# Kernel tuning notes

Hardware: AMD Instinct MI355X
Metric: run time of the kernel (lower is better)

Reference implementation:

```python
import jax, jax.numpy as jnp
import numpy as np

BLOCK = 32            # MX block size (base-class default)
FMT_MAX = 1.984375    # MXINT8 element max = 127/64 (concrete _quantize_elements choice)
QSTEP = 64.0          # quantization grid step 2^-6
BUDGET = 8.0          # cfg.msd_cycle_budget
THRESH = 0.0          # cfg.msd_budget_dynamic_threshold
ALPHA = 1.0           # cfg.msd_budget_dynamic_scale (mode='linear')
NEG = -60.0           # log2 sentinel for zero/negative values


def _safe_log2(x):
    return jnp.where(x > 0, jnp.log2(jnp.maximum(x, 1e-45)), NEG)


def _quantize_blocks(t):
    """Per-block shared fp32 scale + MXINT8-style element quantization.
    t: (rows, feat) with feat % BLOCK == 0 -> q (rows, nb, bs), scales (rows, nb)."""
    rows = t.shape[0]
    blocks = t.reshape(rows, -1, BLOCK)
    max_abs = jnp.max(jnp.abs(blocks), axis=-1)
    scales = jnp.maximum(max_abs / FMT_MAX, 1e-30)
    q = jnp.round(blocks / scales[..., None] * QSTEP) / QSTEP
    return q, scales


def _msd_truncate(value, num_digits):
    """Truncate each element to its num_digits most-significant NAF (BSD) digits."""
    abs_v = jnp.abs(value)
    sign = jnp.sign(value)
    mask = (num_digits > 0) & (abs_v > 0)
    msb_pos = jnp.floor(jnp.log2(jnp.maximum(abs_v, 1e-45)))
    scale_up = jnp.exp2(23.0 - msb_pos)              # place MSB at bit 23
    x_scaled = jnp.round(abs_v * scale_up).astype(jnp.int32)
    x_h = x_scaled >> 1
    s = x_scaled + x_h
    naf_pos = s & ~x_h
    naf_neg = x_h & ~s
    combined = naf_pos | naf_neg
    naf_width = jnp.where(
        combined > 0,
        jnp.floor(jnp.log2(jnp.maximum(combined.astype(jnp.float32), 1.0))).astype(jnp.int32) + 1,
        jnp.zeros_like(combined),
    )
    drop = jnp.clip(naf_width - num_digits.astype(jnp.int32), 0, 31)
    keep_mask = ~((jnp.int32(1) << drop) - 1)
    recon = ((naf_pos & keep_mask).astype(jnp.float32)
             - (naf_neg & keep_mask).astype(jnp.float32)) / scale_up
    return jnp.where(mask, sign * recon, jnp.zeros_like(recon))


def _forward(x, weight, bias):
    x_q, x_scales = _quantize_blocks(x)        # (N, nb, bs), (N, nb)
    w_q, w_scales = _quantize_blocks(weight)   # (O, nb, bs), (O, nb)
    # inter-block delays from shared scales
    combined_e = jnp.floor(_safe_log2(x_scales)[:, None, :]
                           + _safe_log2(w_scales)[None, :, :])   # (N, O, nb)
    e_max = jnp.max(combined_e, axis=-1)                         # (N, O)
    inter = e_max[..., None] - combined_e                        # (N, O, nb)
    # intra-block delays from activation element exponents
    abs_q = jnp.abs(x_q)
    elem_e = jnp.where(abs_q > 0, jnp.floor(jnp.log2(jnp.maximum(abs_q, 1e-45))), NEG)
    intra = jnp.max(elem_e, axis=-1, keepdims=True) - elem_e     # (N, nb, bs)
    # hybrid Glocal per-channel cycle budgets (linear dynamic mode)
    b_final = BUDGET + ALPHA * jnp.clip(e_max - THRESH, 0.0)     # (N, O)
    eff = (b_final[:, :, None, None]
           - inter[..., None]
           - intra[:, None, :, :])                               # (N, O, nb, bs)
    prod = x_q[:, None, :, :] * w_q[None, :, :, :]               # (N, O, nb, bs)
    trunc = jax.lax.stop_gradient(_msd_truncate(prod, eff))      # torch.no_grad()
    block_dot = jnp.sum(trunc, axis=-1)                          # (N, O, nb)
    out = jnp.einsum('nb,ob,nob->no', x_scales, w_scales, block_dot)
    return out + bias[None, :]


def setup_inputs() -> dict:
    key = jax.random.key(0)
    k1, k2, k3 = jax.random.split(key, 3)
    N, IN, OUT = 128, 1024, 512
    x = jax.random.normal(k1, (N, IN), dtype=jnp.float32)
    weight = jax.random.normal(k2, (OUT, IN), dtype=jnp.float32) * 0.02
    bias = jax.random.normal(k3, (OUT,), dtype=jnp.float32)
    return {"x": x, "weight": weight, "bias": bias}


def reference(x, weight, bias):
    return _forward(x, weight, bias)
```

## Files before the change

### kernel.cpp

```cpp
#include <hip/hip_runtime.h>
#include <math.h>

#define NROWS 128
#define KDIM  1024
#define ODIM  512
#define NB    32
#define BS    32

__device__ __forceinline__ int clz32(unsigned x) { return x ? __builtin_clz(x) : 32; }

__device__ __forceinline__ int naf_keep(int P, int isum) {
  int kept, h, t, c, dr;
  asm volatile(
      "v_ashrrev_i32 %1, 1, %5\n\t"
      "v_add_u32     %2, %5, %1\n\t"
      "v_xor_b32     %3, %2, %1\n\t"
      "v_or_b32      %3, 1, %3\n\t"
      "v_ffbh_u32    %3, %3\n\t"
      "v_sub_u32     %4, %6, %3\n\t"
      "v_med3_i32    %4, %4, 0, 31\n\t"
      "v_bfe_u32     %3, %2, 0, %4\n\t"
      "v_bfe_u32     %2, %1, 0, %4\n\t"
      "v_sub_u32     %3, %3, %2\n\t"
      "v_sub_u32     %0, %5, %3\n\t"
      : "=v"(kept), "=&v"(h), "=&v"(t), "=&v"(c), "=&v"(dr)
      : "v"(P), "v"(isum));
  return kept;
}

__global__ void prep_kernel(const float* __restrict__ x, const float* __restrict__ wgt,
                            unsigned short* __restrict__ xp, unsigned char* __restrict__ wq,
                            float* __restrict__ xs, float* __restrict__ lxs,
                            float* __restrict__ wsc, float* __restrict__ lws) {
  const int bid = blockIdx.x;
  if (bid < 16) {
    int tid = bid * 256 + threadIdx.x;
    int row = tid >> 5, blk = tid & 31;
    const float4* p = (const float4*)(x + (size_t)row * KDIM + blk * BS);
    float v[32];
    float m = 0.f;
#pragma unroll
    for (int i = 0; i < 8; ++i) {
      float4 f = p[i];
      v[4*i+0] = f.x; v[4*i+1] = f.y; v[4*i+2] = f.z; v[4*i+3] = f.w;
      m = fmaxf(m, fmaxf(fmaxf(fabsf(f.x), fabsf(f.y)), fmaxf(fabsf(f.z), fabsf(f.w))));
    }
    float scale = fmaxf(m / 1.984375f, 1e-30f);
    int q[32], e[32], emax = -60;
#pragma unroll
    for (int i = 0; i < 32; ++i) {
      float t = v[i] / scale * 64.0f;
      int qi = (int)rintf(t);
      q[i] = qi;
      int a = qi < 0 ? -qi : qi;
      int ei = a ? (31 - clz32((unsigned)a)) - 6 : -60;
      e[i] = ei;
      emax = ei > emax ? ei : emax;
    }
    unsigned short u[32];
#pragma unroll
    for (int i = 0; i < 32; ++i)
      u[i] = (unsigned short)(((emax - e[i]) << 8) | (q[i] & 0xFF));
    uint4* dst = (uint4*)(xp + (size_t)row * KDIM + blk * BS);
#pragma unroll
    for (int i = 0; i < 4; ++i) {
      uint4 w4;
      w4.x = (unsigned)u[8*i+0] | ((unsigned)u[8*i+1] << 16);
      w4.y = (unsigned)u[8*i+2] | ((unsigned)u[8*i+3] << 16);
      w4.z = (unsigned)u[8*i+4] | ((unsigned)u[8*i+5] << 16);
      w4.w = (unsigned)u[8*i+6] | ((unsigned)u[8*i+7] << 16);
      dst[i] = w4;
    }
    xs[tid] = scale;
    lxs[tid] = (float)log2((double)scale);
  } else {
    int tid = (bid - 16) * 256 + threadIdx.x;
    int row = tid >> 5, blk = tid & 31;
    const float4* p = (const float4*)(wgt + (size_t)row * KDIM + blk * BS);
    float v[32];
    float m = 0.f;
#pragma unroll
    for (int i = 0; i < 8; ++i) {
      float4 f = p[i];
      v[4*i+0] = f.x; v[4*i+1] = f.y; v[4*i+2] = f.z; v[4*i+3] = f.w;
      m = fmaxf(m, fmaxf(fmaxf(fabsf(f.x), fabsf(f.y)), fmaxf(fabsf(f.z), fabsf(f.w))));
    }
    float scale = fmaxf(m / 1.984375f, 1e-30f);
    unsigned char c[32];
#pragma unroll
    for (int i = 0; i < 32; ++i) {
      float t = v[i] / scale * 64.0f;
      int qi = (int)rintf(t);
      c[i] = (unsigned char)(qi & 0xFF);
    }
    uint4* dst = (uint4*)(wq + (size_t)row * KDIM + blk * BS);
#pragma unroll
    for (int i = 0; i < 2; ++i) {
      uint4 w4;
      w4.x = (unsigned)c[16*i+ 0] | ((unsigned)c[16*i+ 1] << 8) | ((unsigned)c[16*i+ 2] << 16) | ((unsigned)c[16*i+ 3] << 24);
      w4.y = (unsigned)c[16*i+ 4] | ((unsigned)c[16*i+ 5] << 8) | ((unsigned)c[16*i+ 6] << 16) | ((unsigned)c[16*i+ 7] << 24);
      w4.z = (unsigned)c[16*i+ 8] | ((unsigned)c[16*i+ 9] << 8) | ((unsigned)c[16*i+10] << 16) | ((unsigned)c[16*i+11] << 24);
      w4.w = (unsigned)c[16*i+12] | ((unsigned)c[16*i+13] << 8) | ((unsigned)c[16*i+14] << 16) | ((unsigned)c[16*i+15] << 24);
      dst[i] = w4;
    }
    wsc[tid] = scale;
    lws[tid] = (float)log2((double)scale);
  }
}

__global__ __launch_bounds__(1024, 8)
void msd_main_kernel(const unsigned short* __restrict__ xp,
                     const unsigned char* __restrict__ wq,
                     const float* __restrict__ xs, const float* __restrict__ lxs,
                     const float* __restrict__ wsc, const float* __restrict__ lws,
                     const float* __restrict__ bias, float* __restrict__ out) {
  __shared__ unsigned short sx[8][1032];
  __shared__ unsigned char  swq[16][1040];
  __shared__ float sxs[8][33], slx[8][33], sws[16][33], slw[16][33];
  __shared__ float sred[7 * 128];
  const int tid = threadIdx.x;
  const int n0 = blockIdx.x * 8, o0 = blockIdx.y * 16;

  {
    int r = tid >> 7, c = tid & 127;
    uint4 d = ((const uint4*)(xp + (size_t)(n0 + r) * KDIM))[c];
    *(uint4*)&sx[r][c * 8] = d;
  }
  {
    int r = tid >> 6, c = tid & 63;
    uint4 d = ((const uint4*)(wq + (size_t)(o0 + r) * KDIM))[c];
    *(uint4*)&swq[r][c * 16] = d;
  }
  {
    int r = tid >> 5, b = tid & 31;
    if (tid < 256) {
      sxs[r][b] = xs[(n0 + r) * NB + b];
      slx[r][b] = lxs[(n0 + r) * NB + b];
    }
    if (tid < 512) {
      sws[r][b] = wsc[(o0 + r) * NB + b];
      slw[r][b] = lws[(o0 + r) * NB + b];
    }
  }
  __syncthreads();

  const int kh = tid >> 7, idx = tid & 127, tn = idx >> 4, to = idx & 15;

  float emf = -1e30f;
#pragma unroll
  for (int b = 0; b < NB; ++b)
    emf = fmaxf(emf, floorf(slx[tn][b] + slw[to][b]));
  const int iemax = (int)emf;
  const int sbase = 24 + (iemax < 0 ? iemax : 0);

  float facc = 0.f;
  const int b0 = kh * 4;
#pragma unroll 1
  for (int bb = 0; bb < 4; ++bb) {
    const int b = b0 + bb;
    const int ice = (int)floorf(slx[tn][b] + slw[to][b]);
    const int s = sbase - ice;
    uint4 xv0 = *(const uint4*)&sx[tn][b * 32 + 0];
    uint4 xv1 = *(const uint4*)&sx[tn][b * 32 + 8];
    uint4 xv2 = *(const uint4*)&sx[tn][b * 32 + 16];
    uint4 xv3 = *(const uint4*)&sx[tn][b * 32 + 24];
    unsigned xd[16] = {xv0.x, xv0.y, xv0.z, xv0.w, xv1.x, xv1.y, xv1.z, xv1.w,
                       xv2.x, xv2.y, xv2.z, xv2.w, xv3.x, xv3.y, xv3.z, xv3.w};
    uint4 wv0 = *(const uint4*)&swq[to][b * 32];
    uint4 wv1 = *(const uint4*)&swq[to][b * 32 + 16];
    unsigned wb[8] = {wv0.x, wv0.y, wv0.z, wv0.w, wv1.x, wv1.y, wv1.z, wv1.w};
    int bacc = 0;
#pragma unroll
    for (int j = 0; j < 16; ++j) {
      const unsigned xw = xd[j];
      const unsigned ww = wb[j >> 1];
      const int ix0 = __builtin_amdgcn_sbfe((int)xw, 0, 8);
      const int in0 = (int)__builtin_amdgcn_ubfe(xw, 8, 8);
      const int ix1 = __builtin_amdgcn_sbfe((int)xw, 16, 8);
      const int in1 = (int)(xw >> 24);
      int iw0, iw1;
      if (j & 1) { iw0 = __builtin_amdgcn_sbfe((int)ww, 16, 8);
                   iw1 = __builtin_amdgcn_sbfe((int)ww, 24, 8); }
      else       { iw0 = __builtin_amdgcn_sbfe((int)ww, 0, 8);
                   iw1 = __builtin_amdgcn_sbfe((int)ww, 8, 8); }
      bacc += naf_keep(__mul24(ix0, iw0), in0 + s);
      bacc += naf_keep(__mul24(ix1, iw1), in1 + s);
    }
    facc += sxs[tn][b] * sws[to][b] * (float)bacc;
  }

  if (kh) sred[(kh - 1) * 128 + idx] = facc;
  __syncthreads();
  if (!kh) {
    float r = facc;
#pragma unroll
    for (int p = 0; p < 7; ++p) r += sred[p * 128 + idx];
    r = r * (1.0f / 4096.0f) + bias[o0 + to];
    out[(size_t)(n0 + tn) * ODIM + (o0 + to)] = r;
  }
}

extern "C" void kernel_launch(void* const* d_in, const int* in_sizes, int n_in,
                              void* d_out, int out_size, void* d_ws, size_t ws_size,
                              hipStream_t stream) {
  const float* x    = (const float*)d_in[0];
  const float* wgt  = (const float*)d_in[1];
  const float* bias = (const float*)d_in[2];
  float* out = (float*)d_out;
  char* ws = (char*)d_ws;
  unsigned short* xp  = (unsigned short*)(ws + 0);
  unsigned char*  wq  = (unsigned char*)(ws + 262144);
  float* xs  = (float*)(ws + 786432);
  float* lxs = (float*)(ws + 802816);
  float* wsc = (float*)(ws + 819200);
  float* lws = (float*)(ws + 884736);

  hipLaunchKernelGGL(prep_kernel, dim3(80), dim3(256), 0, stream,
                     x, wgt, xp, wq, xs, lxs, wsc, lws);
  hipLaunchKernelGGL(msd_main_kernel, dim3(16, 32), dim3(1024), 0, stream,
                     xp, wq, xs, lxs, wsc, lws, bias, out);
}
```

Baseline: 37.31 us.

## Fuse quantization prep into main MSD kernel, dropping workspace round-trip

Removes the separate prep kernel and quantizes x and weight blocks directly into shared memory inside the main kernel, with each block recomputing the scales and packed codes for its tile. This eliminates one kernel launch and the global workspace write/read. In exchange, the quantization work is redundantly recomputed across the grid: each x tile is requantized by 32 blocks and each weight tile by 16 blocks. Only 768 of the 1024 threads take part in the prologue, and it adds fp32 global reads and divisions before the main loop.

```diff
diff --git a/kernel.cpp b/kernel.cpp
--- a/kernel.cpp
+++ b/kernel.cpp
@@ -28,92 +28,9 @@
   return kept;
 }
 
-__global__ void prep_kernel(const float* __restrict__ x, const float* __restrict__ wgt,
-                            unsigned short* __restrict__ xp, unsigned char* __restrict__ wq,
-                            float* __restrict__ xs, float* __restrict__ lxs,
-                            float* __restrict__ wsc, float* __restrict__ lws) {
-  const int bid = blockIdx.x;
-  if (bid < 16) {
-    int tid = bid * 256 + threadIdx.x;
-    int row = tid >> 5, blk = tid & 31;
-    const float4* p = (const float4*)(x + (size_t)row * KDIM + blk * BS);
-    float v[32];
-    float m = 0.f;
-#pragma unroll
-    for (int i = 0; i < 8; ++i) {
-      float4 f = p[i];
-      v[4*i+0] = f.x; v[4*i+1] = f.y; v[4*i+2] = f.z; v[4*i+3] = f.w;
-      m = fmaxf(m, fmaxf(fmaxf(fabsf(f.x), fabsf(f.y)), fmaxf(fabsf(f.z), fabsf(f.w))));
-    }
-    float scale = fmaxf(m / 1.984375f, 1e-30f);
-    int q[32], e[32], emax = -60;
-#pragma unroll
-    for (int i = 0; i < 32; ++i) {
-      float t = v[i] / scale * 64.0f;
-      int qi = (int)rintf(t);
-      q[i] = qi;
-      int a = qi < 0 ? -qi : qi;
-      int ei = a ? (31 - clz32((unsigned)a)) - 6 : -60;
-      e[i] = ei;
-      emax = ei > emax ? ei : emax;
-    }
-    unsigned short u[32];
-#pragma unroll
-    for (int i = 0; i < 32; ++i)
-      u[i] = (unsigned short)(((emax - e[i]) << 8) | (q[i] & 0xFF));
-    uint4* dst = (uint4*)(xp + (size_t)row * KDIM + blk * BS);
-#pragma unroll
-    for (int i = 0; i < 4; ++i) {
-      uint4 w4;
-      w4.x = (unsigned)u[8*i+0] | ((unsigned)u[8*i+1] << 16);
-      w4.y = (unsigned)u[8*i+2] | ((unsigned)u[8*i+3] << 16);
-      w4.z = (unsigned)u[8*i+4] | ((unsigned)u[8*i+5] << 16);
-      w4.w = (unsigned)u[8*i+6] | ((unsigned)u[8*i+7] << 16);
-      dst[i] = w4;
-    }
-    xs[tid] = scale;
-    lxs[tid] = (float)log2((double)scale);
-  } else {
-    int tid = (bid - 16) * 256 + threadIdx.x;
-    int row = tid >> 5, blk = tid & 31;
-    const float4* p = (const float4*)(wgt + (size_t)row * KDIM + blk * BS);
-    float v[32];
-    float m = 0.f;
-#pragma unroll
-    for (int i = 0; i < 8; ++i) {
-      float4 f = p[i];
-      v[4*i+0] = f.x; v[4*i+1] = f.y; v[4*i+2] = f.z; v[4*i+3] = f.w;
-      m = fmaxf(m, fmaxf(fmaxf(fabsf(f.x), fabsf(f.y)), fmaxf(fabsf(f.z), fabsf(f.w))));
-    }
-    float scale = fmaxf(m / 1.984375f, 1e-30f);
-    unsigned char c[32];
-#pragma unroll
-    for (int i = 0; i < 32; ++i) {
-      float t = v[i] / scale * 64.0f;
-      int qi = (int)rintf(t);
-      c[i] = (unsigned char)(qi & 0xFF);
-    }
-    uint4* dst = (uint4*)(wq + (size_t)row * KDIM + blk * BS);
-#pragma unroll
-    for (int i = 0; i < 2; ++i) {
-      uint4 w4;
-      w4.x = (unsigned)c[16*i+ 0] | ((unsigned)c[16*i+ 1] << 8) | ((unsigned)c[16*i+ 2] << 16) | ((unsigned)c[16*i+ 3] << 24);
-      w4.y = (unsigned)c[16*i+ 4] | ((unsigned)c[16*i+ 5] << 8) | ((unsigned)c[16*i+ 6] << 16) | ((unsigned)c[16*i+ 7] << 24);
-      w4.z = (unsigned)c[16*i+ 8] | ((unsigned)c[16*i+ 9] << 8) | ((unsigned)c[16*i+10] << 16) | ((unsigned)c[16*i+11] << 24);
-      w4.w = (unsigned)c[16*i+12] | ((unsigned)c[16*i+13] << 8) | ((unsigned)c[16*i+14] << 16) | ((unsigned)c[16*i+15] << 24);
-      dst[i] = w4;
-    }
-    wsc[tid] = scale;
-    lws[tid] = (float)log2((double)scale);
-  }
-}
-
 __global__ __launch_bounds__(1024, 8)
-void msd_main_kernel(const unsigned short* __restrict__ xp,
-                     const unsigned char* __restrict__ wq,
-                     const float* __restrict__ xs, const float* __restrict__ lxs,
-                     const float* __restrict__ wsc, const float* __restrict__ lws,
-                     const float* __restrict__ bias, float* __restrict__ out) {
+void msd_fused_kernel(const float* __restrict__ x, const float* __restrict__ wgt,
+                      const float* __restrict__ bias, float* __restrict__ out) {
   __shared__ unsigned short sx[8][1032];
   __shared__ unsigned char  swq[16][1040];
   __shared__ float sxs[8][33], slx[8][33], sws[16][33], slw[16][33];
@@ -121,26 +38,78 @@
   const int tid = threadIdx.x;
   const int n0 = blockIdx.x * 8, o0 = blockIdx.y * 16;
 
-  {
-    int r = tid >> 7, c = tid & 127;
-    uint4 d = ((const uint4*)(xp + (size_t)(n0 + r) * KDIM))[c];
-    *(uint4*)&sx[r][c * 8] = d;
-  }
-  {
-    int r = tid >> 6, c = tid & 63;
-    uint4 d = ((const uint4*)(wq + (size_t)(o0 + r) * KDIM))[c];
-    *(uint4*)&swq[r][c * 16] = d;
-  }
-  {
-    int r = tid >> 5, b = tid & 31;
-    if (tid < 256) {
-      sxs[r][b] = xs[(n0 + r) * NB + b];
-      slx[r][b] = lxs[(n0 + r) * NB + b];
+  if (tid < 256) {
+    const int r = tid >> 5, b = tid & 31;
+    const float4* p = (const float4*)(x + (size_t)(n0 + r) * KDIM + b * BS);
+    float4 f[8];
+    float m = 0.f;
+#pragma unroll
+    for (int i = 0; i < 8; ++i) {
+      f[i] = p[i];
+      m = fmaxf(m, fmaxf(fmaxf(fabsf(f[i].x), fabsf(f[i].y)),
+                         fmaxf(fabsf(f[i].z), fabsf(f[i].w))));
     }
-    if (tid < 512) {
-      sws[r][b] = wsc[(o0 + r) * NB + b];
-      slw[r][b] = lws[(o0 + r) * NB + b];
+    const float scale = fmaxf(m / 1.984375f, 1e-30f);
+    unsigned uw[16];
+    int emax = -60;
+#pragma unroll
+    for (int i = 0; i < 32; ++i) {
+      const float vi = (i & 3) == 0 ? f[i >> 2].x
+                     : (i & 3) == 1 ? f[i >> 2].y
+                     : (i & 3) == 2 ? f[i >> 2].z : f[i >> 2].w;
+      float t = vi / scale * 64.0f;
+      int qi = (int)rintf(t);
+      int a = qi < 0 ? -qi : qi;
+      int ei = a ? (31 - clz32((unsigned)a)) - 6 : -60;
+      emax = ei > emax ? ei : emax;
+      unsigned entry = (((unsigned)(ei + 60)) << 8) | ((unsigned)qi & 0xFFu);
+      if ((i & 1) == 0) uw[i >> 1] = entry;
+      else              uw[i >> 1] |= entry << 16;
     }
+    const unsigned emax60 = (unsigned)(emax + 60);
+#pragma unroll
+    for (int g = 0; g < 4; ++g) {
+      unsigned wd[4];
+#pragma unroll
+      for (int k = 0; k < 4; ++k) {
+        const unsigned w = uw[g * 4 + k];
+        const unsigned lo = ((emax60 - ((w >> 8) & 0xFFu)) << 8) | (w & 0xFFu);
+        const unsigned hi = ((emax60 - (w >> 24)) << 8) | ((w >> 16) & 0xFFu);
+        wd[k] = lo | (hi << 16);
+      }
+      *(uint4*)&sx[r][b * 32 + g * 8] = make_uint4(wd[0], wd[1], wd[2], wd[3]);
+    }
+    sxs[r][b] = scale;
+    slx[r][b] = (float)log2((double)scale);
+  } else if (tid < 768) {
+    const int t2 = tid - 256;
+    const int r = t2 >> 5, b = t2 & 31;
+    const float4* p = (const float4*)(wgt + (size_t)(o0 + r) * KDIM + b * BS);
+    float4 f[8];
+    float m = 0.f;
+#pragma unroll
+    for (int i = 0; i < 8; ++i) {
+      f[i] = p[i];
+      m = fmaxf(m, fmaxf(fmaxf(fabsf(f[i].x), fabsf(f[i].y)),
+                         fmaxf(fabsf(f[i].z), fabsf(f[i].w))));
+    }
+    const float scale = fmaxf(m / 1.984375f, 1e-30f);
+    unsigned cw[8];
+#pragma unroll
+    for (int i = 0; i < 32; ++i) {
+      const float vi = (i & 3) == 0 ? f[i >> 2].x
+                     : (i & 3) == 1 ? f[i >> 2].y
+                     : (i & 3) == 2 ? f[i >> 2].z : f[i >> 2].w;
+      float t = vi / scale * 64.0f;
+      int qi = (int)rintf(t);
+      unsigned byte = (unsigned)qi & 0xFFu;
+      if ((i & 3) == 0) cw[i >> 2] = byte;
+      else              cw[i >> 2] |= byte << (8 * (i & 3));
+    }
+    *(uint4*)&swq[r][b * 32]      = make_uint4(cw[0], cw[1], cw[2], cw[3]);
+    *(uint4*)&swq[r][b * 32 + 16] = make_uint4(cw[4], cw[5], cw[6], cw[7]);
+    sws[r][b] = scale;
+    slw[r][b] = (float)log2((double)scale);
   }
   __syncthreads();
 
@@ -207,16 +176,8 @@
   const float* wgt  = (const float*)d_in[1];
   const float* bias = (const float*)d_in[2];
   float* out = (float*)d_out;
-  char* ws = (char*)d_ws;
-  unsigned short* xp  = (unsigned short*)(ws + 0);
-  unsigned char*  wq  = (unsigned char*)(ws + 262144);
-  float* xs  = (float*)(ws + 786432);
-  float* lxs = (float*)(ws + 802816);
-  float* wsc = (float*)(ws + 819200);
-  float* lws = (float*)(ws + 884736);
+  (void)d_ws; (void)ws_size;
 
-  hipLaunchKernelGGL(prep_kernel, dim3(80), dim3(256), 0, stream,
-                     x, wgt, xp, wq, xs, lxs, wsc, lws);
-  hipLaunchKernelGGL(msd_main_kernel, dim3(16, 32), dim3(1024), 0, stream,
-                     xp, wq, xs, lxs, wsc, lws, bias, out);
+  hipLaunchKernelGGL(msd_fused_kernel, dim3(16, 32), dim3(1024), 0, stream,
+                     x, wgt, bias, out);
 }
```

New measurement: 40.39 us. +8.2%, slower.
